# Optimization experiments

Measured on AMD Instinct MI355X. Metric: run time of the kernel, lower is better.

The kernel has to match this reference:

```python
import jax, jax.numpy as jnp
import numpy as np

D_MODEL = 2048
R = 32
LN_EPS = 1e-5  # torch nn.LayerNorm default


def setup_inputs() -> dict:
    key = jax.random.key(0)
    k_x, k_wd, k_wu = jax.random.split(key, 3)
    x = jax.random.normal(k_x, (4, 4096, D_MODEL), dtype=jnp.float32)
    gamma = jnp.ones((D_MODEL,), dtype=jnp.float32)
    beta = jnp.zeros((D_MODEL,), dtype=jnp.float32)
    # down: default torch Linear init ~ U(-1/sqrt(d), 1/sqrt(d)); approximate with scaled normal
    w_down = jax.random.normal(k_wd, (D_MODEL, R), dtype=jnp.float32) / jnp.sqrt(jnp.float32(D_MODEL))
    b_down = jnp.zeros((R,), dtype=jnp.float32)
    # up: nn.init.normal_(std=0.001), bias zero
    w_up = jax.random.normal(k_wu, (R, D_MODEL), dtype=jnp.float32) * 0.001
    b_up = jnp.zeros((D_MODEL,), dtype=jnp.float32)
    return {"x": x, "gamma": gamma, "beta": beta, "w_down": w_down,
            "b_down": b_down, "w_up": w_up, "b_up": b_up}


def reference(x, gamma, beta, w_down, b_down, w_up, b_up):
    # LayerNorm over last dim
    mu = jnp.mean(x, axis=-1, keepdims=True)
    var = jnp.mean(jnp.square(x - mu), axis=-1, keepdims=True)
    h = (x - mu) * jax.lax.rsqrt(var + LN_EPS) * gamma + beta
    # down-proj -> exact GELU (torch nn.GELU default) -> up-proj -> residual
    h = jnp.einsum('bsd,dr->bsr', h, w_down) + b_down
    h = jax.nn.gelu(h, approximate=False)
    h = jnp.einsum('bsr,rd->bsd', h, w_up) + b_up
    return x + h
```

## Files before the change

### kernel.cpp

```cpp
#include <hip/hip_runtime.h>
#include <math.h>

#define D     2048
#define NR    32
#define ROWS  16

typedef short bf16x8 __attribute__((ext_vector_type(8)));
typedef float f32x4  __attribute__((ext_vector_type(4)));

__device__ __forceinline__ unsigned int f2bf(float f) {
    unsigned int u = __float_as_uint(f);
    return (u + 0x7FFFu + ((u >> 16) & 1u)) >> 16;
}
__device__ __forceinline__ unsigned int pk2(float a, float b) {
    return f2bf(a) | (f2bf(b) << 16);
}

__global__ __launch_bounds__(64)
void k_prep(const float* __restrict__ wd, const float* __restrict__ gamma,
            const float* __restrict__ beta, const float* __restrict__ wu,
            unsigned int* __restrict__ wuf, unsigned int* __restrict__ wdpf,
            float* __restrict__ c12p)
{
    const int l = threadIdx.x;
    const int q = l >> 4, p = l & 15;
    const int b = blockIdx.x;
    if (b < 128) {
        const int t = b;
        float v[8];
        #pragma unroll
        for (int e = 0; e < 8; ++e)
            v[e] = wu[(q * 8 + e) * D + t * 16 + p];
        uint4 pk;
        pk.x = pk2(v[0], v[1]); pk.y = pk2(v[2], v[3]);
        pk.z = pk2(v[4], v[5]); pk.w = pk2(v[6], v[7]);
        *(uint4*)&wuf[(t * 64 + l) * 4] = pk;
    } else {
        const int idx = b - 128;
        const int kk = idx >> 1, n = idx & 1;
        const int r = n * 16 + p;
        float wv[8];
        float c1 = 0.f, c2 = 0.f;
        #pragma unroll
        for (int e = 0; e < 8; ++e) {
            const int k = kk * 32 + q * 8 + e;
            const float wdv = wd[k * NR + r];
            wv[e] = gamma[k] * wdv;
            c1 += wv[e];
            c2 += beta[k] * wdv;
        }
        uint4 pk;
        pk.x = pk2(wv[0], wv[1]); pk.y = pk2(wv[2], wv[3]);
        pk.z = pk2(wv[4], wv[5]); pk.w = pk2(wv[6], wv[7]);
        *(uint4*)&wdpf[(idx * 64 + l) * 4] = pk;
        c1 += __shfl_xor(c1, 16); c1 += __shfl_xor(c1, 32);
        c2 += __shfl_xor(c2, 16); c2 += __shfl_xor(c2, 32);
        if (q == 0) {
            c12p[idx * 32 + p]      = c1;
            c12p[idx * 32 + 16 + p] = c2;
        }
    }
}

__global__ __launch_bounds__(64)
void k_c12(const float* __restrict__ c12p, float* __restrict__ c12)
{
    const int i = threadIdx.x;
    const int half = i >> 5, r = i & 31;
    const int n = r >> 4, rr = r & 15;
    float s = 0.f;
    for (int kk = 0; kk < 64; ++kk)
        s += c12p[(kk * 2 + n) * 32 + half * 16 + rr];
    c12[i] = s;
}

__global__ __launch_bounds__(512, 4)
void k_fused(const float* __restrict__ x, const float* __restrict__ bd,
             const float* __restrict__ bu, const unsigned int* __restrict__ wuf,
             const unsigned int* __restrict__ wdpf, const float* __restrict__ c12,
             float* __restrict__ out)
{
    __shared__ unsigned int xs[ROWS * 1024];
    __shared__ float Sp[8][16][16];
    __shared__ unsigned short a_sh[ROWS][NR];
    __shared__ float mu_s[ROWS], rs_s[ROWS];

    const int tid = threadIdx.x;
    const int w = tid >> 6, l = tid & 63;
    const int p = l & 15, q = l >> 4;
    const long row0 = (long)blockIdx.x * ROWS;

    #pragma unroll
    for (int rp = 0; rp < 2; ++rp) {
        const int row = w * 2 + rp;
        const float* xr = x + (row0 + row) * D;
        float s = 0.f, s2 = 0.f;
        #pragma unroll
        for (int it = 0; it < 8; ++it) {
            const int j = it * 256 + l * 4;
            float4 v = *(const float4*)(xr + j);
            uint2 pkk;
            pkk.x = pk2(v.x, v.y);
            pkk.y = pk2(v.z, v.w);
            const int byte = (row * 4096 + j * 2) ^ (row << 4);
            *(uint2*)((char*)xs + byte) = pkk;
            s  += v.x + v.y + v.z + v.w;
            s2 += v.x * v.x + v.y * v.y + v.z * v.z + v.w * v.w;
        }
        #pragma unroll
        for (int off = 32; off >= 1; off >>= 1) {
            s  += __shfl_xor(s, off);
            s2 += __shfl_xor(s2, off);
        }
        if (l == 0) {
            const float mu  = s * (1.0f / D);
            const float var = s2 * (1.0f / D) - mu * mu;
            mu_s[row] = mu;
            rs_s[row] = rsqrtf(var + 1e-5f);
        }
    }
    __syncthreads();

    {
        const int ks = w & 3, n = w >> 2;
        f32x4 acc = {0.f, 0.f, 0.f, 0.f};
        #pragma unroll 4
        for (int t = 0; t < 16; ++t) {
            const int byte = (p * 4096 + (ks * 512 + t * 32) * 2 + q * 16) ^ (p << 4);
            const bf16x8 af = *(const bf16x8*)((const char*)xs + byte);
            const int kk = ks * 16 + t;
            const bf16x8 bf = *(const bf16x8*)&wdpf[(kk * 2 + n) * 256 + l * 4];
            acc = __builtin_amdgcn_mfma_f32_16x16x32_bf16(af, bf, acc, 0, 0, 0);
        }
        *(f32x4*)&Sp[w][p][q * 4] = acc;
    }
    __syncthreads();

    {
        const int m = tid >> 5, r = tid & 31;
        const int n = r >> 4, rr = r & 15;
        const float S = Sp[4 * n + 0][rr][m] + Sp[4 * n + 1][rr][m]
                      + Sp[4 * n + 2][rr][m] + Sp[4 * n + 3][rr][m];
        const float y = rs_s[m] * (S - mu_s[m] * c12[r]) + c12[32 + r] + bd[r];
        const float a = 0.5f * y * (1.0f + erff(y * 0.70710678118654752f));
        a_sh[m][r] = (unsigned short)f2bf(a);
    }
    __syncthreads();

    {
        const bf16x8 afc = *(const bf16x8*)((const char*)a_sh + p * 64 + q * 16);
        const long xbase = (row0 + p) * D;
        const f32x4 z = {0.f, 0.f, 0.f, 0.f};
        #pragma unroll 4
        for (int t = 0; t < 16; ++t) {
            const int j0 = w * 256 + t * 16;
            const bf16x8 bw = *(const bf16x8*)&wuf[(w * 16 + t) * 256 + l * 4];
            f32x4 dd = __builtin_amdgcn_mfma_f32_16x16x32_bf16(bw, afc, z, 0, 0, 0);
            const int jj = j0 + q * 4;
            const float4 xv = *(const float4*)(x + xbase + jj);
            const float4 bv = *(const float4*)(bu + jj);
            f32x4 o;
            o[0] = xv.x + bv.x + dd[0];
            o[1] = xv.y + bv.y + dd[1];
            o[2] = xv.z + bv.z + dd[2];
            o[3] = xv.w + bv.w + dd[3];
            __builtin_nontemporal_store(o, (f32x4*)(out + xbase + jj));
        }
    }
}

extern "C" void kernel_launch(void* const* d_in, const int* in_sizes, int n_in,
                              void* d_out, int out_size, void* d_ws, size_t ws_size,
                              hipStream_t stream) {
    (void)n_in; (void)ws_size; (void)out_size;
    const float* x     = (const float*)d_in[0];
    const float* gamma = (const float*)d_in[1];
    const float* beta  = (const float*)d_in[2];
    const float* wd    = (const float*)d_in[3];
    const float* bd    = (const float*)d_in[4];
    const float* wu    = (const float*)d_in[5];
    const float* bu    = (const float*)d_in[6];
    float* out = (float*)d_out;

    unsigned int* wuf  = (unsigned int*)d_ws;
    unsigned int* wdpf = wuf + 32768;
    float* c12p = (float*)(wdpf + 32768);
    float* c12  = c12p + 4096;

    const int nrows  = in_sizes[0] / D;
    const int blocks = nrows / ROWS;

    hipLaunchKernelGGL(k_prep,  dim3(256),    dim3(64),  0, stream,
                       wd, gamma, beta, wu, wuf, wdpf, c12p);
    hipLaunchKernelGGL(k_c12,   dim3(1),      dim3(64),  0, stream, c12p, c12);
    hipLaunchKernelGGL(k_fused, dim3(blocks), dim3(512), 0, stream,
                       x, bd, bu, wuf, wdpf, c12, out);
}
```

Measured before the change: 274.3 us.

## Split fused adapter into down-projection and up-projection kernels, dropping LDS staging

The single fused kernel is split into two kernels. The first streams x straight from global memory into registers, converts it to bf16 and feeds the MFMA directly, computing LayerNorm statistics on the fly with no LDS staging of the whole row tile. It then writes the GELU activations as packed bf16 to a workspace. The second kernel reads those activations and recomputes the up-projection plus the residual. The split frees the 64KB of LDS per block and should raise occupancy, but x is now read twice from global memory and there is an extra launch.

```diff
diff --git a/kernel.cpp b/kernel.cpp
--- a/kernel.cpp
+++ b/kernel.cpp
@@ -3,7 +3,6 @@
 
 #define D     2048
 #define NR    32
-#define ROWS  16
 
 typedef short bf16x8 __attribute__((ext_vector_type(8)));
 typedef float f32x4  __attribute__((ext_vector_type(4)));
@@ -74,98 +73,100 @@
     c12[i] = s;
 }
 
-__global__ __launch_bounds__(512, 4)
-void k_fused(const float* __restrict__ x, const float* __restrict__ bd,
-             const float* __restrict__ bu, const unsigned int* __restrict__ wuf,
+__global__ __launch_bounds__(256, 4)
+void k1_down(const float* __restrict__ x, const float* __restrict__ bd,
              const unsigned int* __restrict__ wdpf, const float* __restrict__ c12,
-             float* __restrict__ out)
-{
-    __shared__ unsigned int xs[ROWS * 1024];
-    __shared__ float Sp[8][16][16];
-    __shared__ unsigned short a_sh[ROWS][NR];
-    __shared__ float mu_s[ROWS], rs_s[ROWS];
+             unsigned int* __restrict__ a_pk)
+{
+    __shared__ float Sp[4][2][16][16];
+    __shared__ float sred[4][16][2];
 
     const int tid = threadIdx.x;
     const int w = tid >> 6, l = tid & 63;
     const int p = l & 15, q = l >> 4;
-    const long row0 = (long)blockIdx.x * ROWS;
-
-    #pragma unroll
-    for (int rp = 0; rp < 2; ++rp) {
-        const int row = w * 2 + rp;
-        const float* xr = x + (row0 + row) * D;
-        float s = 0.f, s2 = 0.f;
-        #pragma unroll
-        for (int it = 0; it < 8; ++it) {
-            const int j = it * 256 + l * 4;
-            float4 v = *(const float4*)(xr + j);
-            uint2 pkk;
-            pkk.x = pk2(v.x, v.y);
-            pkk.y = pk2(v.z, v.w);
-            const int byte = (row * 4096 + j * 2) ^ (row << 4);
-            *(uint2*)((char*)xs + byte) = pkk;
-            s  += v.x + v.y + v.z + v.w;
-            s2 += v.x * v.x + v.y * v.y + v.z * v.z + v.w * v.w;
-        }
-        #pragma unroll
-        for (int off = 32; off >= 1; off >>= 1) {
-            s  += __shfl_xor(s, off);
-            s2 += __shfl_xor(s2, off);
-        }
-        if (l == 0) {
-            const float mu  = s * (1.0f / D);
-            const float var = s2 * (1.0f / D) - mu * mu;
-            mu_s[row] = mu;
-            rs_s[row] = rsqrtf(var + 1e-5f);
-        }
-    }
+    const long row0 = (long)blockIdx.x * 16;
+
+    const float* xr = x + (row0 + p) * D + w * 512 + q * 8;
+    f32x4 acc0 = {0.f, 0.f, 0.f, 0.f}, acc1 = {0.f, 0.f, 0.f, 0.f};
+    float s = 0.f, s2 = 0.f;
+
+    #pragma unroll 4
+    for (int t = 0; t < 16; ++t) {
+        const float4 v0 = *(const float4*)(xr + t * 32);
+        const float4 v1 = *(const float4*)(xr + t * 32 + 4);
+        s  += v0.x + v0.y + v0.z + v0.w + v1.x + v1.y + v1.z + v1.w;
+        s2 += v0.x * v0.x + v0.y * v0.y + v0.z * v0.z + v0.w * v0.w
+            + v1.x * v1.x + v1.y * v1.y + v1.z * v1.z + v1.w * v1.w;
+        union { uint4 u; bf16x8 h; } cvt;
+        cvt.u.x = pk2(v0.x, v0.y); cvt.u.y = pk2(v0.z, v0.w);
+        cvt.u.z = pk2(v1.x, v1.y); cvt.u.w = pk2(v1.z, v1.w);
+        const int kk = w * 16 + t;
+        const bf16x8 b0 = *(const bf16x8*)&wdpf[(kk * 2 + 0) * 256 + l * 4];
+        const bf16x8 b1 = *(const bf16x8*)&wdpf[(kk * 2 + 1) * 256 + l * 4];
+        acc0 = __builtin_amdgcn_mfma_f32_16x16x32_bf16(cvt.h, b0, acc0, 0, 0, 0);
+        acc1 = __builtin_amdgcn_mfma_f32_16x16x32_bf16(cvt.h, b1, acc1, 0, 0, 0);
+    }
+
+    s  += __shfl_xor(s, 16);  s  += __shfl_xor(s, 32);
+    s2 += __shfl_xor(s2, 16); s2 += __shfl_xor(s2, 32);
+    if (q == 0) { sred[w][p][0] = s; sred[w][p][1] = s2; }
+    *(f32x4*)&Sp[w][0][p][q * 4] = acc0;
+    *(f32x4*)&Sp[w][1][p][q * 4] = acc1;
     __syncthreads();
 
     {
-        const int ks = w & 3, n = w >> 2;
-        f32x4 acc = {0.f, 0.f, 0.f, 0.f};
-        #pragma unroll 4
-        for (int t = 0; t < 16; ++t) {
-            const int byte = (p * 4096 + (ks * 512 + t * 32) * 2 + q * 16) ^ (p << 4);
-            const bf16x8 af = *(const bf16x8*)((const char*)xs + byte);
-            const int kk = ks * 16 + t;
-            const bf16x8 bf = *(const bf16x8*)&wdpf[(kk * 2 + n) * 256 + l * 4];
-            acc = __builtin_amdgcn_mfma_f32_16x16x32_bf16(af, bf, acc, 0, 0, 0);
-        }
-        *(f32x4*)&Sp[w][p][q * 4] = acc;
-    }
-    __syncthreads();
-
-    {
-        const int m = tid >> 5, r = tid & 31;
-        const int n = r >> 4, rr = r & 15;
-        const float S = Sp[4 * n + 0][rr][m] + Sp[4 * n + 1][rr][m]
-                      + Sp[4 * n + 2][rr][m] + Sp[4 * n + 3][rr][m];
-        const float y = rs_s[m] * (S - mu_s[m] * c12[r]) + c12[32 + r] + bd[r];
-        const float a = 0.5f * y * (1.0f + erff(y * 0.70710678118654752f));
-        a_sh[m][r] = (unsigned short)f2bf(a);
-    }
-    __syncthreads();
-
-    {
-        const bf16x8 afc = *(const bf16x8*)((const char*)a_sh + p * 64 + q * 16);
-        const long xbase = (row0 + p) * D;
-        const f32x4 z = {0.f, 0.f, 0.f, 0.f};
-        #pragma unroll 4
-        for (int t = 0; t < 16; ++t) {
-            const int j0 = w * 256 + t * 16;
-            const bf16x8 bw = *(const bf16x8*)&wuf[(w * 16 + t) * 256 + l * 4];
-            f32x4 dd = __builtin_amdgcn_mfma_f32_16x16x32_bf16(bw, afc, z, 0, 0, 0);
-            const int jj = j0 + q * 4;
-            const float4 xv = *(const float4*)(x + xbase + jj);
-            const float4 bv = *(const float4*)(bu + jj);
-            f32x4 o;
-            o[0] = xv.x + bv.x + dd[0];
-            o[1] = xv.y + bv.y + dd[1];
-            o[2] = xv.z + bv.z + dd[2];
-            o[3] = xv.w + bv.w + dd[3];
-            __builtin_nontemporal_store(o, (f32x4*)(out + xbase + jj));
-        }
+        const int m = tid >> 4, rp = tid & 15;
+        float ssum = 0.f, s2sum = 0.f;
+        #pragma unroll
+        for (int ww = 0; ww < 4; ++ww) {
+            ssum  += sred[ww][m][0];
+            s2sum += sred[ww][m][1];
+        }
+        const float mu   = ssum * (1.0f / D);
+        const float var  = s2sum * (1.0f / D) - mu * mu;
+        const float rstd = rsqrtf(var + 1e-5f);
+        float av[2];
+        #pragma unroll
+        for (int i = 0; i < 2; ++i) {
+            const int r = rp * 2 + i;
+            const int n = r >> 4, rr = r & 15;
+            const float S = Sp[0][n][rr][m] + Sp[1][n][rr][m]
+                          + Sp[2][n][rr][m] + Sp[3][n][rr][m];
+            const float y = rstd * (S - mu * c12[r]) + c12[32 + r] + bd[r];
+            av[i] = 0.5f * y * (1.0f + erff(y * 0.70710678118654752f));
+        }
+        a_pk[(row0 + m) * 16 + rp] = pk2(av[0], av[1]);
+    }
+}
+
+__global__ __launch_bounds__(256, 4)
+void k2_up(const float* __restrict__ x, const unsigned int* __restrict__ a_pk,
+           const unsigned int* __restrict__ wuf, const float* __restrict__ bu,
+           float* __restrict__ out)
+{
+    const int tid = threadIdx.x;
+    const int w = tid >> 6, l = tid & 63;
+    const int p = l & 15, q = l >> 4;
+    const long row0 = (long)blockIdx.x * 16;
+
+    const bf16x8 afc = *(const bf16x8*)&a_pk[(row0 + p) * 16 + q * 4];
+    const long xbase = (row0 + p) * D;
+    const f32x4 z = {0.f, 0.f, 0.f, 0.f};
+
+    #pragma unroll 4
+    for (int t = 0; t < 32; ++t) {
+        const int jt = w * 32 + t;
+        const int jj = jt * 16 + q * 4;
+        const bf16x8 bw = *(const bf16x8*)&wuf[jt * 256 + l * 4];
+        f32x4 dd = __builtin_amdgcn_mfma_f32_16x16x32_bf16(bw, afc, z, 0, 0, 0);
+        const float4 xv = *(const float4*)(x + xbase + jj);
+        const float4 bv = *(const float4*)(bu + jj);
+        f32x4 o;
+        o[0] = xv.x + bv.x + dd[0];
+        o[1] = xv.y + bv.y + dd[1];
+        o[2] = xv.z + bv.z + dd[2];
+        o[3] = xv.w + bv.w + dd[3];
+        __builtin_nontemporal_store(o, (f32x4*)(out + xbase + jj));
     }
 }
 
@@ -186,13 +187,16 @@
     unsigned int* wdpf = wuf + 32768;
     float* c12p = (float*)(wdpf + 32768);
     float* c12  = c12p + 4096;
+    unsigned int* a_pk = (unsigned int*)(c12 + 64);
 
     const int nrows  = in_sizes[0] / D;
-    const int blocks = nrows / ROWS;
-
-    hipLaunchKernelGGL(k_prep,  dim3(256),    dim3(64),  0, stream,
+    const int tiles  = nrows / 16;
+
+    hipLaunchKernelGGL(k_prep,  dim3(256),   dim3(64),  0, stream,
                        wd, gamma, beta, wu, wuf, wdpf, c12p);
-    hipLaunchKernelGGL(k_c12,   dim3(1),      dim3(64),  0, stream, c12p, c12);
-    hipLaunchKernelGGL(k_fused, dim3(blocks), dim3(512), 0, stream,
-                       x, bd, bu, wuf, wdpf, c12, out);
-}
+    hipLaunchKernelGGL(k_c12,   dim3(1),     dim3(64),  0, stream, c12p, c12);
+    hipLaunchKernelGGL(k1_down, dim3(tiles), dim3(256), 0, stream,
+                       x, bd, wdpf, c12, a_pk);
+    hipLaunchKernelGGL(k2_up,   dim3(tiles), dim3(256), 0, stream,
+                       x, a_pk, wuf, bu, out);
+}
```

Result: no change. 273.1 us (-0.4%).
